# Optimization experiments

Hardware: AMD Instinct MI355X
Metric: run time of the kernel (lower is better)

Reference implementation:

```python
import jax, jax.numpy as jnp
import numpy as np


def setup_inputs() -> dict:
    key = jax.random.key(0)
    k1, k2, k3, k4, k5 = jax.random.split(key, 5)
    n_nodes, input_dim, hidden1 = 100000, 512, 128
    z_dim = hidden1 // 2
    n_edges = 1000000
    X = jax.random.normal(k1, (n_nodes, input_dim), dtype=jnp.float32)
    W = jax.random.normal(k2, (input_dim, hidden1), dtype=jnp.float32) * 0.05
    W2 = jax.random.normal(k3, (hidden1, z_dim), dtype=jnp.float32) * 0.05
    train_edges = jax.random.randint(k4, (n_edges, 2), 0, n_nodes, dtype=jnp.int64)
    train_false_edges = jax.random.randint(k5, (n_edges, 2), 0, n_nodes, dtype=jnp.int64)
    return {"X": X, "W": W, "W2": W2,
            "train_edges": train_edges, "train_false_edges": train_false_edges}


def _decode(z, edges):
    # fused gather -> elementwise mult -> row sum over all edges at once
    # z: [N, d], edges: [E, 2] -> [E, 1]
    return jnp.sum(z[edges[:, 0]] * z[edges[:, 1]], axis=-1, keepdims=True)


def reference(X, W, W2, train_edges, train_false_edges):
    # encode: note torch.mm(adj, x) in the original is dead code; output is
    # activation(x @ W), so adj never affects the result.
    h = jax.nn.relu(X @ W)          # [N, hidden1]
    z = h @ W2                      # [N, z_dim] (identity activation)
    z1 = _decode(z, train_edges)        # [E, 1]
    z2 = _decode(z, train_false_edges)  # [E, 1]
    return jax.nn.sigmoid(jnp.concatenate([z1, z2], axis=0))  # [2E, 1]
```

## Files before the change

kernel.cpp:

```cpp
#include <hip/hip_runtime.h>
#include <hip/hip_bf16.h>
#include <hip/hip_fp16.h>
#include <math.h>

#define IN_DIM 512
#define H1     128
#define ZD     64

#define NBKT   128
#define BCAP   18432

typedef __attribute__((ext_vector_type(8))) short bf16x8;
typedef __attribute__((ext_vector_type(4))) float f32x4;

__device__ __forceinline__ ushort f32_to_bf16_bits(float x) {
    unsigned b = __float_as_uint(x);
    unsigned r = (b + 0x7FFF + ((b >> 16) & 1)) >> 16;
    return (ushort)r;
}

__global__ void prepack_w(const float* __restrict__ W,
                          ushort* __restrict__ Whi, ushort* __restrict__ Wlo,
                          int* __restrict__ cursors) {
    if (blockIdx.x == 0 && threadIdx.x < NBKT)
        cursors[threadIdx.x] = threadIdx.x * BCAP;

    int t = blockIdx.x * 256 + threadIdx.x;
    int s  = t >> 9;
    int cb = (t >> 6) & 7;
    int l  = t & 63;
    ushort h[8], lo[8];
    #pragma unroll
    for (int j = 0; j < 8; ++j) {
        int k   = s * 32 + ((l >> 4) * 8) + j;
        int col = cb * 16 + (l & 15);
        float x = W[(size_t)k * H1 + col];
        ushort hb = f32_to_bf16_bits(x);
        float  hf = __uint_as_float((unsigned)hb << 16);
        h[j]  = hb;
        lo[j] = f32_to_bf16_bits(x - hf);
    }
    size_t off = ((size_t)t) * 8;
    *(ushort4*)&Whi[off]     = make_ushort4(h[0], h[1], h[2], h[3]);
    *(ushort4*)&Whi[off + 4] = make_ushort4(h[4], h[5], h[6], h[7]);
    *(ushort4*)&Wlo[off]     = make_ushort4(lo[0], lo[1], lo[2], lo[3]);
    *(ushort4*)&Wlo[off + 4] = make_ushort4(lo[4], lo[5], lo[6], lo[7]);
}

__global__ __launch_bounds__(256, 4) void encode_kernel(
    const float* __restrict__ X, const ushort* __restrict__ Whi,
    const ushort* __restrict__ Wlo, const float* __restrict__ W2,
    __half* __restrict__ Z, int N)
{
    __shared__ __align__(16) union {
        ushort st[2][2][4][512];
        __half ht[H1][72];
    } sm;

    const int tid  = threadIdx.x;
    const int lane = tid & 63;
    const int w    = tid >> 6;
    const int wr   = w >> 1;
    const int wc   = w & 1;
    const int row0 = blockIdx.x * 64;

    const int srb  = tid >> 6;
    const int sla  = tid & 63;
    const int srow = srb * 16 + (tid & 15);
    const int kq   = (tid >> 4) & 3;
    const bool srow_ok = (row0 + srow) < N;
    const float* xp = X + (size_t)(row0 + srow) * IN_DIM + kq * 8;

    f32x4 acc[2][4];
    #pragma unroll
    for (int i = 0; i < 2; ++i)
        #pragma unroll
        for (int j = 0; j < 4; ++j) acc[i][j] = (f32x4){0.f, 0.f, 0.f, 0.f};

    float4 rgA, rgB;
    rgA = srow_ok ? *(const float4*)(xp + 0) : make_float4(0, 0, 0, 0);
    rgB = srow_ok ? *(const float4*)(xp + 4) : make_float4(0, 0, 0, 0);

    auto stage = [&](int buf) {
        float xv[8] = {rgA.x, rgA.y, rgA.z, rgA.w, rgB.x, rgB.y, rgB.z, rgB.w};
        unsigned hb[8], lb[8];
        #pragma unroll
        for (int j = 0; j < 8; ++j) {
            unsigned b = __float_as_uint(xv[j]);
            unsigned hf = b & 0xFFFF0000u;
            hb[j] = b;
            lb[j] = __float_as_uint(xv[j] - __uint_as_float(hf));
        }
        uint4 hp, lp;
        hp.x = (hb[0] >> 16) | (hb[1] & 0xFFFF0000u);
        hp.y = (hb[2] >> 16) | (hb[3] & 0xFFFF0000u);
        hp.z = (hb[4] >> 16) | (hb[5] & 0xFFFF0000u);
        hp.w = (hb[6] >> 16) | (hb[7] & 0xFFFF0000u);
        lp.x = (lb[0] >> 16) | (lb[1] & 0xFFFF0000u);
        lp.y = (lb[2] >> 16) | (lb[3] & 0xFFFF0000u);
        lp.z = (lb[4] >> 16) | (lb[5] & 0xFFFF0000u);
        lp.w = (lb[6] >> 16) | (lb[7] & 0xFFFF0000u);
        *(uint4*)&sm.st[buf][0][srb][sla * 8] = hp;
        *(uint4*)&sm.st[buf][1][srb][sla * 8] = lp;
    };

    stage(0);
    rgA = srow_ok ? *(const float4*)(xp + 32) : make_float4(0, 0, 0, 0);
    rgB = srow_ok ? *(const float4*)(xp + 36) : make_float4(0, 0, 0, 0);
    __syncthreads();

    for (int s = 0; s < 16; ++s) {
        const int buf = s & 1;
        bf16x8 aH[2], aL[2];
        #pragma unroll
        for (int rb = 0; rb < 2; ++rb) {
            int rbg = wr * 2 + rb;
            aH[rb] = *(const bf16x8*)&sm.st[buf][0][rbg][lane * 8];
            aL[rb] = *(const bf16x8*)&sm.st[buf][1][rbg][lane * 8];
        }
        if (s < 15) stage(buf ^ 1);
        if (s < 14) {
            const float* xp2 = xp + (s + 2) * 32;
            rgA = srow_ok ? *(const float4*)(xp2 + 0) : make_float4(0, 0, 0, 0);
            rgB = srow_ok ? *(const float4*)(xp2 + 4) : make_float4(0, 0, 0, 0);
        }
        #pragma unroll
        for (int cb = 0; cb < 4; ++cb) {
            int cbg = wc * 4 + cb;
            size_t off = ((size_t)(s * 8 + cbg) * 64 + lane) * 8;
            bf16x8 bH = *(const bf16x8*)&Whi[off];
            bf16x8 bL = *(const bf16x8*)&Wlo[off];
            #pragma unroll
            for (int rb = 0; rb < 2; ++rb) {
                acc[rb][cb] = __builtin_amdgcn_mfma_f32_16x16x32_bf16(
                    aH[rb], bH, acc[rb][cb], 0, 0, 0);
                acc[rb][cb] = __builtin_amdgcn_mfma_f32_16x16x32_bf16(
                    aH[rb], bL, acc[rb][cb], 0, 0, 0);
                acc[rb][cb] = __builtin_amdgcn_mfma_f32_16x16x32_bf16(
                    aL[rb], bH, acc[rb][cb], 0, 0, 0);
            }
        }
        __syncthreads();
    }

    #pragma unroll
    for (int rb = 0; rb < 2; ++rb)
        #pragma unroll
        for (int cb = 0; cb < 4; ++cb) {
            int col = wc * 64 + cb * 16 + (lane & 15);
            int rr  = wr * 32 + rb * 16 + (lane >> 4) * 4;
            *(__half2*)&sm.ht[col][rr] =
                __floats2half2_rn(fmaxf(acc[rb][cb][0], 0.f), fmaxf(acc[rb][cb][1], 0.f));
            *(__half2*)&sm.ht[col][rr + 2] =
                __floats2half2_rn(fmaxf(acc[rb][cb][2], 0.f), fmaxf(acc[rb][cb][3], 0.f));
        }
    __syncthreads();

    const int tx = tid & 31;
    const int ty = tid >> 5;

    float zacc[8][2];
    #pragma unroll
    for (int i = 0; i < 8; ++i) { zacc[i][0] = 0.f; zacc[i][1] = 0.f; }

    #pragma unroll 4
    for (int k = 0; k < H1; ++k) {
        float2 b = *(const float2*)&W2[(size_t)k * ZD + tx * 2];
        union { uint4 u; __half2 h[4]; } hv;
        hv.u = *(const uint4*)&sm.ht[k][ty * 8];
        #pragma unroll
        for (int q = 0; q < 4; ++q) {
            float2 fa = __half22float2(hv.h[q]);
            zacc[2 * q][0]     = fmaf(fa.x, b.x, zacc[2 * q][0]);
            zacc[2 * q][1]     = fmaf(fa.x, b.y, zacc[2 * q][1]);
            zacc[2 * q + 1][0] = fmaf(fa.y, b.x, zacc[2 * q + 1][0]);
            zacc[2 * q + 1][1] = fmaf(fa.y, b.y, zacc[2 * q + 1][1]);
        }
    }
    #pragma unroll
    for (int i = 0; i < 8; ++i) {
        int gr = row0 + ty * 8 + i;
        if (gr < N)
            *(__half2*)&Z[(size_t)gr * ZD + tx * 2] =
                __floats2half2_rn(zacc[i][0], zacc[i][1]);
    }
}

__global__ __launch_bounds__(256) void scatter_kernel(
    const int* __restrict__ e1, const int* __restrict__ e2,
    int4* __restrict__ recs, int* __restrict__ cursors, int E, float invA, float invB)
{
    __shared__ int lhist[NBKT];
    __shared__ int lcur[NBKT];
    const int tid = threadIdx.x;
    const int total = 2 * E;
    const int chunk = (total + gridDim.x - 1) / gridDim.x;
    const int start = blockIdx.x * chunk;
    const int end   = min(start + chunk, total);

    for (int i = tid; i < NBKT; i += 256) lhist[i] = 0;
    __syncthreads();

    for (int i = start + tid; i < end; i += 256) {
        int2 ab = (i < E) ? *(const int2*)&e1[2 * (size_t)i]
                          : *(const int2*)&e2[2 * (size_t)(i - E)];
        int as = min((int)(ab.x * invA), 7);
        int bs = min((int)(ab.y * invB), 15);
        atomicAdd(&lhist[as * 16 + bs], 1);
    }
    __syncthreads();
    for (int i = tid; i < NBKT; i += 256)
        lcur[i] = atomicAdd(&cursors[i], lhist[i]);
    __syncthreads();

    for (int i = start + tid; i < end; i += 256) {
        int2 ab = (i < E) ? *(const int2*)&e1[2 * (size_t)i]
                          : *(const int2*)&e2[2 * (size_t)(i - E)];
        int as = min((int)(ab.x * invA), 7);
        int bs = min((int)(ab.y * invB), 15);
        int bkt = as * 16 + bs;
        int pos = atomicAdd(&lcur[bkt], 1);
        if (pos < (bkt + 1) * BCAP)
            recs[pos] = make_int4(ab.x, ab.y, i, 0);
    }
}

__global__ __launch_bounds__(256) void decode_sorted(
    const __half* __restrict__ Zh, const int4* __restrict__ recs,
    const int* __restrict__ cursors, float* __restrict__ out)
{
    const int k = blockIdx.x & 7;
    const int t = blockIdx.x >> 3;
    const int tid  = threadIdx.x;
    const int lane = tid & 63;
    const int wv   = tid >> 6;
    const int sub  = lane >> 3;
    const int l    = lane & 7;
    const int slot = t * 32 + wv * 8 + sub;

    #pragma unroll 1
    for (int j = 0; j < 16; ++j) {
        const int p = k * 16 + j;
        const int start = p * BCAP;
        const int end   = min(cursors[p], start + BCAP);
        for (int r = start + slot; r < end; r += 8192) {
            int4 rec = recs[r];
            union { uint4 u; __half2 h[4]; } A, B;
            A.u = *(const uint4*)&Zh[(size_t)rec.x * ZD + l * 8];
            B.u = *(const uint4*)&Zh[(size_t)rec.y * ZD + l * 8];
            float s = 0.f;
            #pragma unroll
            for (int q = 0; q < 4; ++q) {
                float2 fa = __half22float2(A.h[q]);
                float2 fb = __half22float2(B.h[q]);
                s += fa.x * fb.x + fa.y * fb.y;
            }
            s += __shfl_xor(s, 4, 64);
            s += __shfl_xor(s, 2, 64);
            s += __shfl_xor(s, 1, 64);
            if (l == 0) out[rec.z] = 1.f / (1.f + __expf(-s));
        }
    }
}

__global__ __launch_bounds__(256) void decode_kernel(
    const __half* __restrict__ Zh, const int* __restrict__ e1,
    const int* __restrict__ e2, float* __restrict__ out, int E)
{
    const int tid  = threadIdx.x;
    const int lane = tid & 63;
    const int wv   = tid >> 6;
    const int sub  = lane >> 3;
    const int l    = lane & 7;
    const int total = 2 * E;
    const int stride = gridDim.x * 32;

    for (int idx = (blockIdx.x * 4 + wv) * 8 + sub; idx < total; idx += stride) {
        const int* ep = (idx < E) ? (e1 + 2 * (size_t)idx)
                                  : (e2 + 2 * (size_t)(idx - E));
        int2 ab = *(const int2*)ep;
        union { uint4 u; __half2 h[4]; } A, B;
        A.u = *(const uint4*)&Zh[(size_t)ab.x * ZD + l * 8];
        B.u = *(const uint4*)&Zh[(size_t)ab.y * ZD + l * 8];
        float s = 0.f;
        #pragma unroll
        for (int q = 0; q < 4; ++q) {
            float2 fa = __half22float2(A.h[q]);
            float2 fb = __half22float2(B.h[q]);
            s += fa.x * fb.x + fa.y * fb.y;
        }
        s += __shfl_xor(s, 4, 64);
        s += __shfl_xor(s, 2, 64);
        s += __shfl_xor(s, 1, 64);
        if (l == 0) out[idx] = 1.f / (1.f + __expf(-s));
    }
}

extern "C" void kernel_launch(void* const* d_in, const int* in_sizes, int n_in,
                              void* d_out, int out_size, void* d_ws, size_t ws_size,
                              hipStream_t stream) {
    const float* X  = (const float*)d_in[0];
    const float* W  = (const float*)d_in[1];
    const float* W2 = (const float*)d_in[2];
    const int*   e1 = (const int*)d_in[3];
    const int*   e2 = (const int*)d_in[4];
    float* out = (float*)d_out;

    const int N = in_sizes[0] / IN_DIM;
    const int E = in_sizes[3] / 2;

    const size_t ZH_OFF  = 0;
    const size_t WHI_OFF = 12800000;
    const size_t WLO_OFF = WHI_OFF + 131072;
    const size_t CUR_OFF = WLO_OFF + 131072;
    const size_t REC_OFF = CUR_OFF + 512;
    const size_t NEEDED  = REC_OFF + (size_t)NBKT * BCAP * 16;

    __half* Zh  = (__half*)((char*)d_ws + ZH_OFF);
    ushort* Whi = (ushort*)((char*)d_ws + WHI_OFF);
    ushort* Wlo = (ushort*)((char*)d_ws + WLO_OFF);
    int*    cur = (int*)((char*)d_ws + CUR_OFF);
    int4*   rec = (int4*)((char*)d_ws + REC_OFF);

    prepack_w<<<32, 256, 0, stream>>>(W, Whi, Wlo, cur);

    const int nblk = (N + 63) / 64;
    encode_kernel<<<nblk, 256, 0, stream>>>(X, Whi, Wlo, W2, Zh, N);

    if (ws_size >= NEEDED) {
        float invA = 8.0f / (float)N;
        float invB = 16.0f / (float)N;
        scatter_kernel<<<256, 256, 0, stream>>>(e1, e2, rec, cur, E, invA, invB);
        decode_sorted<<<2048, 256, 0, stream>>>(Zh, rec, cur, out);
    } else {
        decode_kernel<<<2048, 256, 0, stream>>>(Zh, e1, e2, out, E);
    }
}
```

Before: 442.1 us.

## Switch encoder to fp16 split MFMA, 128-row tiles, packed records, dynamic XCC-aware decode queue

The encoder now converts X to a single fp16 term with round-toward-zero conversion and drops the third (low-times-high) MFMA. W is still kept as an fp16 hi/lo pair. The row tile per block doubles to 128, with launch bounds lowered to 3 blocks per CU. Edge records shrink from 16-byte int4 to packed 8-byte u64, cutting scatter and decode traffic. The decode kernel reads the XCC id and pulls 128-record chunks from per-XCC atomic queues for load balancing. The trade-offs are reduced X precision (fp16 range and rtz error), atomic queue contention, and reliance on N < 2^17 for the packed node indices.

```diff
diff --git a/kernel.cpp b/kernel.cpp
--- a/kernel.cpp
+++ b/kernel.cpp
@@ -1,5 +1,4 @@
 #include <hip/hip_runtime.h>
-#include <hip/hip_bf16.h>
 #include <hip/hip_fp16.h>
 #include <math.h>
 
@@ -9,22 +8,22 @@
 
 #define NBKT   128
 #define BCAP   18432
-
-typedef __attribute__((ext_vector_type(8))) short bf16x8;
-typedef __attribute__((ext_vector_type(4))) float f32x4;
-
-__device__ __forceinline__ ushort f32_to_bf16_bits(float x) {
-    unsigned b = __float_as_uint(x);
-    unsigned r = (b + 0x7FFF + ((b >> 16) & 1)) >> 16;
-    return (ushort)r;
-}
+#define QCH    128
+#define CPB    144
+#define ROWPAD 136
+
+typedef __attribute__((ext_vector_type(8))) short  f16x8;
+typedef __attribute__((ext_vector_type(4))) float  f32x4;
+typedef __fp16 fp16x2 __attribute__((ext_vector_type(2)));
+typedef unsigned long long u64;
 
 __global__ void prepack_w(const float* __restrict__ W,
                           ushort* __restrict__ Whi, ushort* __restrict__ Wlo,
-                          int* __restrict__ cursors) {
-    if (blockIdx.x == 0 && threadIdx.x < NBKT)
-        cursors[threadIdx.x] = threadIdx.x * BCAP;
-
+                          int* __restrict__ cur, int* __restrict__ qcur) {
+    if (blockIdx.x == 0) {
+        if (threadIdx.x < NBKT) cur[threadIdx.x] = threadIdx.x * BCAP;
+        if (threadIdx.x >= NBKT && threadIdx.x < NBKT + 8) qcur[threadIdx.x - NBKT] = 0;
+    }
     int t = blockIdx.x * 256 + threadIdx.x;
     int s  = t >> 9;
     int cb = (t >> 6) & 7;
@@ -35,10 +34,10 @@
         int k   = s * 32 + ((l >> 4) * 8) + j;
         int col = cb * 16 + (l & 15);
         float x = W[(size_t)k * H1 + col];
-        ushort hb = f32_to_bf16_bits(x);
-        float  hf = __uint_as_float((unsigned)hb << 16);
-        h[j]  = hb;
-        lo[j] = f32_to_bf16_bits(x - hf);
+        __half hh = __float2half(x);
+        __half hl = __float2half(x - __half2float(hh));
+        h[j]  = __half_as_ushort(hh);
+        lo[j] = __half_as_ushort(hl);
     }
     size_t off = ((size_t)t) * 8;
     *(ushort4*)&Whi[off]     = make_ushort4(h[0], h[1], h[2], h[3]);
@@ -47,14 +46,14 @@
     *(ushort4*)&Wlo[off + 4] = make_ushort4(lo[4], lo[5], lo[6], lo[7]);
 }
 
-__global__ __launch_bounds__(256, 4) void encode_kernel(
+__global__ __launch_bounds__(256, 3) void encode_kernel(
     const float* __restrict__ X, const ushort* __restrict__ Whi,
     const ushort* __restrict__ Wlo, const float* __restrict__ W2,
     __half* __restrict__ Z, int N)
 {
     __shared__ __align__(16) union {
-        ushort st[2][2][4][512];
-        __half ht[H1][72];
+        ushort st[2][8][512];
+        __half ht[H1][ROWPAD];
     } sm;
 
     const int tid  = threadIdx.x;
@@ -62,93 +61,84 @@
     const int w    = tid >> 6;
     const int wr   = w >> 1;
     const int wc   = w & 1;
-    const int row0 = blockIdx.x * 64;
-
-    const int srb  = tid >> 6;
-    const int sla  = tid & 63;
-    const int srow = srb * 16 + (tid & 15);
-    const int kq   = (tid >> 4) & 3;
-    const bool srow_ok = (row0 + srow) < N;
-    const float* xp = X + (size_t)(row0 + srow) * IN_DIM + kq * 8;
-
-    f32x4 acc[2][4];
-    #pragma unroll
-    for (int i = 0; i < 2; ++i)
+    const int row0 = blockIdx.x * 128;
+
+    const int srow = tid >> 2;
+    const int kq   = tid & 3;
+    const int srb0 = srow >> 4;
+    const int srb1 = srb0 + 4;
+    const int sla  = (srow & 15) | (kq << 4);
+    const bool ok0 = (row0 + srow) < N;
+    const bool ok1 = (row0 + srow + 64) < N;
+    const float* xp0 = X + (size_t)(row0 + srow) * IN_DIM + kq * 8;
+    const float* xp1 = X + (size_t)(row0 + srow + 64) * IN_DIM + kq * 8;
+
+    f32x4 acc[4][4];
+    #pragma unroll
+    for (int i = 0; i < 4; ++i)
         #pragma unroll
         for (int j = 0; j < 4; ++j) acc[i][j] = (f32x4){0.f, 0.f, 0.f, 0.f};
 
-    float4 rgA, rgB;
-    rgA = srow_ok ? *(const float4*)(xp + 0) : make_float4(0, 0, 0, 0);
-    rgB = srow_ok ? *(const float4*)(xp + 4) : make_float4(0, 0, 0, 0);
-
+    float4 rg0, rg1, rg2, rg3;
+    const float4 fz = make_float4(0.f, 0.f, 0.f, 0.f);
+    auto loadrg = [&](int s) {
+        const float* p0 = xp0 + s * 32;
+        const float* p1 = xp1 + s * 32;
+        rg0 = ok0 ? *(const float4*)(p0)     : fz;
+        rg1 = ok0 ? *(const float4*)(p0 + 4) : fz;
+        rg2 = ok1 ? *(const float4*)(p1)     : fz;
+        rg3 = ok1 ? *(const float4*)(p1 + 4) : fz;
+    };
     auto stage = [&](int buf) {
-        float xv[8] = {rgA.x, rgA.y, rgA.z, rgA.w, rgB.x, rgB.y, rgB.z, rgB.w};
-        unsigned hb[8], lb[8];
-        #pragma unroll
-        for (int j = 0; j < 8; ++j) {
-            unsigned b = __float_as_uint(xv[j]);
-            unsigned hf = b & 0xFFFF0000u;
-            hb[j] = b;
-            lb[j] = __float_as_uint(xv[j] - __uint_as_float(hf));
-        }
-        uint4 hp, lp;
-        hp.x = (hb[0] >> 16) | (hb[1] & 0xFFFF0000u);
-        hp.y = (hb[2] >> 16) | (hb[3] & 0xFFFF0000u);
-        hp.z = (hb[4] >> 16) | (hb[5] & 0xFFFF0000u);
-        hp.w = (hb[6] >> 16) | (hb[7] & 0xFFFF0000u);
-        lp.x = (lb[0] >> 16) | (lb[1] & 0xFFFF0000u);
-        lp.y = (lb[2] >> 16) | (lb[3] & 0xFFFF0000u);
-        lp.z = (lb[4] >> 16) | (lb[5] & 0xFFFF0000u);
-        lp.w = (lb[6] >> 16) | (lb[7] & 0xFFFF0000u);
-        *(uint4*)&sm.st[buf][0][srb][sla * 8] = hp;
-        *(uint4*)&sm.st[buf][1][srb][sla * 8] = lp;
+        union { fp16x2 h; unsigned u; } c;
+        uint4 w0, w1;
+        c.h = __builtin_amdgcn_cvt_pkrtz(rg0.x, rg0.y); w0.x = c.u;
+        c.h = __builtin_amdgcn_cvt_pkrtz(rg0.z, rg0.w); w0.y = c.u;
+        c.h = __builtin_amdgcn_cvt_pkrtz(rg1.x, rg1.y); w0.z = c.u;
+        c.h = __builtin_amdgcn_cvt_pkrtz(rg1.z, rg1.w); w0.w = c.u;
+        c.h = __builtin_amdgcn_cvt_pkrtz(rg2.x, rg2.y); w1.x = c.u;
+        c.h = __builtin_amdgcn_cvt_pkrtz(rg2.z, rg2.w); w1.y = c.u;
+        c.h = __builtin_amdgcn_cvt_pkrtz(rg3.x, rg3.y); w1.z = c.u;
+        c.h = __builtin_amdgcn_cvt_pkrtz(rg3.z, rg3.w); w1.w = c.u;
+        *(uint4*)&sm.st[buf][srb0][sla * 8] = w0;
+        *(uint4*)&sm.st[buf][srb1][sla * 8] = w1;
     };
 
+    loadrg(0);
     stage(0);
-    rgA = srow_ok ? *(const float4*)(xp + 32) : make_float4(0, 0, 0, 0);
-    rgB = srow_ok ? *(const float4*)(xp + 36) : make_float4(0, 0, 0, 0);
+    loadrg(1);
     __syncthreads();
 
     for (int s = 0; s < 16; ++s) {
         const int buf = s & 1;
-        bf16x8 aH[2], aL[2];
-        #pragma unroll
-        for (int rb = 0; rb < 2; ++rb) {
-            int rbg = wr * 2 + rb;
-            aH[rb] = *(const bf16x8*)&sm.st[buf][0][rbg][lane * 8];
-            aL[rb] = *(const bf16x8*)&sm.st[buf][1][rbg][lane * 8];
-        }
+        f16x8 aH[4];
+        #pragma unroll
+        for (int rb = 0; rb < 4; ++rb)
+            aH[rb] = *(const f16x8*)&sm.st[buf][wr * 4 + rb][lane * 8];
         if (s < 15) stage(buf ^ 1);
-        if (s < 14) {
-            const float* xp2 = xp + (s + 2) * 32;
-            rgA = srow_ok ? *(const float4*)(xp2 + 0) : make_float4(0, 0, 0, 0);
-            rgB = srow_ok ? *(const float4*)(xp2 + 4) : make_float4(0, 0, 0, 0);
-        }
+        if (s < 14) loadrg(s + 2);
         #pragma unroll
         for (int cb = 0; cb < 4; ++cb) {
-            int cbg = wc * 4 + cb;
-            size_t off = ((size_t)(s * 8 + cbg) * 64 + lane) * 8;
-            bf16x8 bH = *(const bf16x8*)&Whi[off];
-            bf16x8 bL = *(const bf16x8*)&Wlo[off];
+            size_t off = ((size_t)(s * 8 + wc * 4 + cb) * 64 + lane) * 8;
+            f16x8 bH = *(const f16x8*)&Whi[off];
+            f16x8 bL = *(const f16x8*)&Wlo[off];
             #pragma unroll
-            for (int rb = 0; rb < 2; ++rb) {
-                acc[rb][cb] = __builtin_amdgcn_mfma_f32_16x16x32_bf16(
+            for (int rb = 0; rb < 4; ++rb) {
+                acc[rb][cb] = __builtin_amdgcn_mfma_f32_16x16x32_f16(
                     aH[rb], bH, acc[rb][cb], 0, 0, 0);
-                acc[rb][cb] = __builtin_amdgcn_mfma_f32_16x16x32_bf16(
+                acc[rb][cb] = __builtin_amdgcn_mfma_f32_16x16x32_f16(
                     aH[rb], bL, acc[rb][cb], 0, 0, 0);
-                acc[rb][cb] = __builtin_amdgcn_mfma_f32_16x16x32_bf16(
-                    aL[rb], bH, acc[rb][cb], 0, 0, 0);
             }
         }
         __syncthreads();
     }
 
     #pragma unroll
-    for (int rb = 0; rb < 2; ++rb)
+    for (int rb = 0; rb < 4; ++rb)
         #pragma unroll
         for (int cb = 0; cb < 4; ++cb) {
             int col = wc * 64 + cb * 16 + (lane & 15);
-            int rr  = wr * 32 + rb * 16 + (lane >> 4) * 4;
+            int rr  = wr * 64 + rb * 16 + (lane >> 4) * 4;
             *(__half2*)&sm.ht[col][rr] =
                 __floats2half2_rn(fmaxf(acc[rb][cb][0], 0.f), fmaxf(acc[rb][cb][1], 0.f));
             *(__half2*)&sm.ht[col][rr + 2] =
@@ -159,27 +149,33 @@
     const int tx = tid & 31;
     const int ty = tid >> 5;
 
-    float zacc[8][2];
-    #pragma unroll
-    for (int i = 0; i < 8; ++i) { zacc[i][0] = 0.f; zacc[i][1] = 0.f; }
-
-    #pragma unroll 4
+    float zacc[16][2];
+    #pragma unroll
+    for (int i = 0; i < 16; ++i) { zacc[i][0] = 0.f; zacc[i][1] = 0.f; }
+
+    #pragma unroll 2
     for (int k = 0; k < H1; ++k) {
         float2 b = *(const float2*)&W2[(size_t)k * ZD + tx * 2];
-        union { uint4 u; __half2 h[4]; } hv;
-        hv.u = *(const uint4*)&sm.ht[k][ty * 8];
+        union { uint4 u; __half2 h[4]; } hv0, hv1;
+        hv0.u = *(const uint4*)&sm.ht[k][ty * 16];
+        hv1.u = *(const uint4*)&sm.ht[k][ty * 16 + 8];
         #pragma unroll
         for (int q = 0; q < 4; ++q) {
-            float2 fa = __half22float2(hv.h[q]);
-            zacc[2 * q][0]     = fmaf(fa.x, b.x, zacc[2 * q][0]);
-            zacc[2 * q][1]     = fmaf(fa.x, b.y, zacc[2 * q][1]);
-            zacc[2 * q + 1][0] = fmaf(fa.y, b.x, zacc[2 * q + 1][0]);
-            zacc[2 * q + 1][1] = fmaf(fa.y, b.y, zacc[2 * q + 1][1]);
-        }
-    }
-    #pragma unroll
-    for (int i = 0; i < 8; ++i) {
-        int gr = row0 + ty * 8 + i;
+            float2 f0 = __half22float2(hv0.h[q]);
+            float2 f1 = __half22float2(hv1.h[q]);
+            zacc[2 * q][0]     = fmaf(f0.x, b.x, zacc[2 * q][0]);
+            zacc[2 * q][1]     = fmaf(f0.x, b.y, zacc[2 * q][1]);
+            zacc[2 * q + 1][0] = fmaf(f0.y, b.x, zacc[2 * q + 1][0]);
+            zacc[2 * q + 1][1] = fmaf(f0.y, b.y, zacc[2 * q + 1][1]);
+            zacc[8 + 2 * q][0]     = fmaf(f1.x, b.x, zacc[8 + 2 * q][0]);
+            zacc[8 + 2 * q][1]     = fmaf(f1.x, b.y, zacc[8 + 2 * q][1]);
+            zacc[8 + 2 * q + 1][0] = fmaf(f1.y, b.x, zacc[8 + 2 * q + 1][0]);
+            zacc[8 + 2 * q + 1][1] = fmaf(f1.y, b.y, zacc[8 + 2 * q + 1][1]);
+        }
+    }
+    #pragma unroll
+    for (int i = 0; i < 16; ++i) {
+        int gr = row0 + ty * 16 + i;
         if (gr < N)
             *(__half2*)&Z[(size_t)gr * ZD + tx * 2] =
                 __floats2half2_rn(zacc[i][0], zacc[i][1]);
@@ -188,7 +184,7 @@
 
 __global__ __launch_bounds__(256) void scatter_kernel(
     const int* __restrict__ e1, const int* __restrict__ e2,
-    int4* __restrict__ recs, int* __restrict__ cursors, int E, float invA, float invB)
+    u64* __restrict__ recs, int* __restrict__ cur, int E, float invA, float invB)
 {
     __shared__ int lhist[NBKT];
     __shared__ int lcur[NBKT];
@@ -210,7 +206,7 @@
     }
     __syncthreads();
     for (int i = tid; i < NBKT; i += 256)
-        lcur[i] = atomicAdd(&cursors[i], lhist[i]);
+        lcur[i] = atomicAdd(&cur[i], lhist[i]);
     __syncthreads();
 
     for (int i = start + tid; i < end; i += 256) {
@@ -221,44 +217,61 @@
         int bkt = as * 16 + bs;
         int pos = atomicAdd(&lcur[bkt], 1);
         if (pos < (bkt + 1) * BCAP)
-            recs[pos] = make_int4(ab.x, ab.y, i, 0);
-    }
-}
-
-__global__ __launch_bounds__(256) void decode_sorted(
-    const __half* __restrict__ Zh, const int4* __restrict__ recs,
-    const int* __restrict__ cursors, float* __restrict__ out)
+            recs[pos] = (u64)(unsigned)ab.x | ((u64)(unsigned)ab.y << 17)
+                      | ((u64)(unsigned)i << 34);
+    }
+}
+
+__global__ __launch_bounds__(256) void decode_q(
+    const __half* __restrict__ Zh, const u64* __restrict__ recs,
+    const int* __restrict__ fill, int* __restrict__ qcur, float* __restrict__ out)
 {
-    const int k = blockIdx.x & 7;
-    const int t = blockIdx.x >> 3;
+    __shared__ int sbase;
+    int myx;
+    asm volatile("s_getreg_b32 %0, hwreg(HW_REG_XCC_ID)" : "=s"(myx));
+    myx &= 7;
+
     const int tid  = threadIdx.x;
     const int lane = tid & 63;
     const int wv   = tid >> 6;
     const int sub  = lane >> 3;
     const int l    = lane & 7;
-    const int slot = t * 32 + wv * 8 + sub;
-
-    #pragma unroll 1
-    for (int j = 0; j < 16; ++j) {
-        const int p = k * 16 + j;
-        const int start = p * BCAP;
-        const int end   = min(cursors[p], start + BCAP);
-        for (int r = start + slot; r < end; r += 8192) {
-            int4 rec = recs[r];
-            union { uint4 u; __half2 h[4]; } A, B;
-            A.u = *(const uint4*)&Zh[(size_t)rec.x * ZD + l * 8];
-            B.u = *(const uint4*)&Zh[(size_t)rec.y * ZD + l * 8];
-            float s = 0.f;
-            #pragma unroll
-            for (int q = 0; q < 4; ++q) {
-                float2 fa = __half22float2(A.h[q]);
-                float2 fb = __half22float2(B.h[q]);
-                s += fa.x * fb.x + fa.y * fb.y;
+    const int slot = wv * 8 + sub;
+
+    for (int xi = 0; xi < 8; ++xi) {
+        const int k = (myx + xi) & 7;
+        while (true) {
+            __syncthreads();
+            if (tid == 0) sbase = atomicAdd(&qcur[k], 1);
+            __syncthreads();
+            int c = sbase;
+            if (c >= 16 * CPB) break;
+            int j   = c / CPB;
+            int off = (c - j * CPB) * QCH;
+            int p    = k * 16 + j;
+            int base = p * BCAP;
+            int lo   = base + off;
+            int hi   = min(min(fill[p], base + BCAP), lo + QCH);
+            for (int r = lo + slot; r < hi; r += 32) {
+                u64 v = recs[r];
+                int a    = (int)(v & 0x1FFFF);
+                int b    = (int)((v >> 17) & 0x1FFFF);
+                int orig = (int)(v >> 34);
+                union { uint4 u; __half2 h[4]; } A, B;
+                A.u = *(const uint4*)&Zh[(size_t)a * ZD + l * 8];
+                B.u = *(const uint4*)&Zh[(size_t)b * ZD + l * 8];
+                float s = 0.f;
+                #pragma unroll
+                for (int q = 0; q < 4; ++q) {
+                    float2 fa = __half22float2(A.h[q]);
+                    float2 fb = __half22float2(B.h[q]);
+                    s += fa.x * fb.x + fa.y * fb.y;
+                }
+                s += __shfl_xor(s, 4, 64);
+                s += __shfl_xor(s, 2, 64);
+                s += __shfl_xor(s, 1, 64);
+                if (l == 0) out[orig] = 1.f / (1.f + __expf(-s));
             }
-            s += __shfl_xor(s, 4, 64);
-            s += __shfl_xor(s, 2, 64);
-            s += __shfl_xor(s, 1, 64);
-            if (l == 0) out[rec.z] = 1.f / (1.f + __expf(-s));
         }
     }
 }
@@ -313,25 +326,27 @@
     const size_t WHI_OFF = 12800000;
     const size_t WLO_OFF = WHI_OFF + 131072;
     const size_t CUR_OFF = WLO_OFF + 131072;
-    const size_t REC_OFF = CUR_OFF + 512;
-    const size_t NEEDED  = REC_OFF + (size_t)NBKT * BCAP * 16;
+    const size_t QQ_OFF  = CUR_OFF + 512;
+    const size_t REC_OFF = QQ_OFF + 512;
+    const size_t NEEDED  = REC_OFF + (size_t)NBKT * BCAP * 8;
 
     __half* Zh  = (__half*)((char*)d_ws + ZH_OFF);
     ushort* Whi = (ushort*)((char*)d_ws + WHI_OFF);
     ushort* Wlo = (ushort*)((char*)d_ws + WLO_OFF);
     int*    cur = (int*)((char*)d_ws + CUR_OFF);
-    int4*   rec = (int4*)((char*)d_ws + REC_OFF);
-
-    prepack_w<<<32, 256, 0, stream>>>(W, Whi, Wlo, cur);
-
-    const int nblk = (N + 63) / 64;
+    int*    qq  = (int*)((char*)d_ws + QQ_OFF);
+    u64*    rec = (u64*)((char*)d_ws + REC_OFF);
+
+    prepack_w<<<32, 256, 0, stream>>>(W, Whi, Wlo, cur, qq);
+
+    const int nblk = (N + 127) / 128;
     encode_kernel<<<nblk, 256, 0, stream>>>(X, Whi, Wlo, W2, Zh, N);
 
     if (ws_size >= NEEDED) {
         float invA = 8.0f / (float)N;
         float invB = 16.0f / (float)N;
         scatter_kernel<<<256, 256, 0, stream>>>(e1, e2, rec, cur, E, invA, invB);
-        decode_sorted<<<2048, 256, 0, stream>>>(Zh, rec, cur, out);
+        decode_q<<<2048, 256, 0, stream>>>(Zh, rec, cur, qq, out);
     } else {
         decode_kernel<<<2048, 256, 0, stream>>>(Zh, e1, e2, out, E);
     }
```

Result: slower. 840.7 us (+90.1%).
